# Performance work log

Hardware: AMD Instinct MI355X
Metric: run time of the kernel (lower is better)

The kernel has to match this reference:

```python
import jax, jax.numpy as jnp
import numpy as np

B, S, D, H = 4, 2048, 1024, 16
DK = D // H  # 64


def setup_inputs() -> dict:
    key = jax.random.key(0)
    ks = jax.random.split(key, 7)
    scale = 1.0 / np.sqrt(D)
    q = jax.random.normal(ks[0], (B, S, D), dtype=jnp.float32)
    k = jax.random.normal(ks[1], (B, S, D), dtype=jnp.float32)
    v = jax.random.normal(ks[2], (B, S, D), dtype=jnp.float32)
    # causal mask, broadcastable to [B, H, S, S]
    mask = jnp.tril(jnp.ones((S, S), dtype=jnp.int32))[None, None, :, :]
    Wq = jax.random.normal(ks[3], (D, D), dtype=jnp.float32) * scale
    Wk = jax.random.normal(ks[4], (D, D), dtype=jnp.float32) * scale
    Wv = jax.random.normal(ks[5], (D, D), dtype=jnp.float32) * scale
    Wo = jax.random.normal(ks[6], (D, D), dtype=jnp.float32) * scale
    return {"q": q, "k": k, "v": v, "mask": mask,
            "Wq": Wq, "Wk": Wk, "Wv": Wv, "Wo": Wo}


def reference(q, k, v, mask, Wq, Wk, Wv, Wo):
    # nn.Linear(bias=False): y = x @ W.T
    query = jnp.einsum('bsd,ed->bse', q, Wq).reshape(B, S, H, DK).transpose(0, 2, 1, 3)
    key_ = jnp.einsum('bsd,ed->bse', k, Wk).reshape(B, S, H, DK).transpose(0, 2, 1, 3)
    value = jnp.einsum('bsd,ed->bse', v, Wv).reshape(B, S, H, DK).transpose(0, 2, 1, 3)
    scores = jnp.einsum('bhqd,bhkd->bhqk', query, key_) / jnp.sqrt(jnp.float32(DK))
    scores = jnp.where(mask == 0, -jnp.inf, scores)
    probs = jax.nn.softmax(scores, axis=-1)
    x = jnp.einsum('bhqk,bhkd->bhqd', probs, value)  # [B,H,S,DK]
    x = x.transpose(0, 2, 1, 3).reshape(B, S, D)
    return jnp.einsum('bsd,ed->bse', x, Wo)
```

## Files before the change

### kernel.cpp

```cpp
#include <hip/hip_runtime.h>
#include <hip/hip_bf16.h>

constexpr int Bn = 4, Sn = 2048, Dn = 1024, Hn = 16, DKn = 64;
constexpr int Mrows = Bn * Sn;
constexpr int NQB = Sn / 64;

typedef __attribute__((ext_vector_type(8))) short short8;
typedef __attribute__((ext_vector_type(4))) float f32x4;
typedef __attribute__((ext_vector_type(4))) unsigned int u32x4;

#define DEV __device__ __forceinline__

DEV unsigned short f2bf(float f) {
    unsigned u = __builtin_bit_cast(unsigned, f);
    u += 0x7FFFu + ((u >> 16) & 1u);
    return (unsigned short)(u >> 16);
}
DEV unsigned pk2(float a, float b) {
    __hip_bfloat162 h = __float22bfloat162_rn(float2{a, b});
    unsigned u;
    __builtin_memcpy(&u, &h, 4);
    return u;
}
DEV float exp2a(float x) {
    float r;
    asm("v_exp_f32 %0, %1" : "=v"(r) : "v"(x));
    return r;
}

__global__ __launch_bounds__(256) void cvt_w(const float* __restrict__ W0,
                                             const float* __restrict__ W1,
                                             const float* __restrict__ W2,
                                             const float* __restrict__ W3,
                                             unsigned short* __restrict__ Out) {
    const float* src = blockIdx.y == 0 ? W0
                     : blockIdx.y == 1 ? W1
                     : blockIdx.y == 2 ? W2 : W3;
    size_t off = ((size_t)blockIdx.x * 256 + threadIdx.x) * 8;
    const float4* s = (const float4*)(src + off);
    float4 a = s[0], b = s[1];
    u32x4 p = {pk2(a.x, a.y), pk2(a.z, a.w), pk2(b.x, b.y), pk2(b.z, b.w)};
    *(u32x4*)(Out + (size_t)blockIdx.y * (Dn * Dn) + off) = p;
}

template <bool ABF16, bool BBF16, bool OUTF32>
DEV void gemm_body(const void* __restrict__ Ap, const void* __restrict__ Bw,
                   void* __restrict__ Out) {
    __shared__ alignas(16) unsigned short As[128 * 40];
    __shared__ alignas(16) unsigned short Bs[128 * 40];

    const int tid = threadIdx.x;
    const int bid = (int)(blockIdx.y * gridDim.x + blockIdx.x);
    const int xcd = bid & 7;
    const int jj = bid >> 3;
    const int m0 = (xcd + ((jj & 7) << 3)) * 128;
    const int n0 = (jj >> 3) * 128;
    const int lane = tid & 63;
    const int w = tid >> 6;
    const int wm = (w >> 1) * 64, wn = (w & 1) * 64;
    const int g = lane >> 4, q15 = lane & 15;

    f32x4 acc[4][4] = {};

    const int srow = tid >> 1, shalf = tid & 1;

    const float* Af = (const float*)Ap;
    const unsigned short* Ab = (const unsigned short*)Ap;
    const float* Bf = (const float*)Bw;
    const unsigned short* Bb = (const unsigned short*)Bw;

    float4 fa0, fa1, fa2, fa3, fb0, fb1, fb2, fb3;
    u32x4 ua0, ua1, ub0, ub1;

    auto loadA = [&](int kk) {
        if constexpr (ABF16) {
            const u32x4* s =
                (const u32x4*)(Ab + (size_t)(m0 + srow) * Dn + kk + shalf * 16);
            ua0 = s[0];
            ua1 = s[1];
        } else {
            const float4* s =
                (const float4*)(Af + (size_t)(m0 + srow) * Dn + kk + shalf * 16);
            fa0 = s[0]; fa1 = s[1]; fa2 = s[2]; fa3 = s[3];
        }
    };
    auto loadB = [&](int kk) {
        if constexpr (BBF16) {
            const u32x4* s =
                (const u32x4*)(Bb + (size_t)(n0 + srow) * Dn + kk + shalf * 16);
            ub0 = s[0];
            ub1 = s[1];
        } else {
            const float4* s =
                (const float4*)(Bf + (size_t)(n0 + srow) * Dn + kk + shalf * 16);
            fb0 = s[0]; fb1 = s[1]; fb2 = s[2]; fb3 = s[3];
        }
    };
    auto store = [&]() {
        u32x4* da = (u32x4*)(&As[srow * 40 + shalf * 16]);
        if constexpr (ABF16) {
            da[0] = ua0;
            da[1] = ua1;
        } else {
            u32x4 p0 = {pk2(fa0.x, fa0.y), pk2(fa0.z, fa0.w), pk2(fa1.x, fa1.y),
                        pk2(fa1.z, fa1.w)};
            u32x4 p1 = {pk2(fa2.x, fa2.y), pk2(fa2.z, fa2.w), pk2(fa3.x, fa3.y),
                        pk2(fa3.z, fa3.w)};
            da[0] = p0;
            da[1] = p1;
        }
        u32x4* db = (u32x4*)(&Bs[srow * 40 + shalf * 16]);
        if constexpr (BBF16) {
            db[0] = ub0;
            db[1] = ub1;
        } else {
            u32x4 q0 = {pk2(fb0.x, fb0.y), pk2(fb0.z, fb0.w), pk2(fb1.x, fb1.y),
                        pk2(fb1.z, fb1.w)};
            u32x4 q1 = {pk2(fb2.x, fb2.y), pk2(fb2.z, fb2.w), pk2(fb3.x, fb3.y),
                        pk2(fb3.z, fb3.w)};
            db[0] = q0;
            db[1] = q1;
        }
    };

    loadA(0);
    loadB(0);
    for (int kk = 0; kk < Dn; kk += 32) {
        store();
        __syncthreads();
        if (kk + 32 < Dn) {
            loadA(kk + 32);
            loadB(kk + 32);
        }

        short8 af[4], bf[4];
#pragma unroll
        for (int mf = 0; mf < 4; ++mf)
            af[mf] = __builtin_bit_cast(
                short8, *(const u32x4*)(&As[(wm + mf * 16 + q15) * 40 + g * 8]));
#pragma unroll
        for (int nf = 0; nf < 4; ++nf)
            bf[nf] = __builtin_bit_cast(
                short8, *(const u32x4*)(&Bs[(wn + nf * 16 + q15) * 40 + g * 8]));
#pragma unroll
        for (int mf = 0; mf < 4; ++mf)
#pragma unroll
            for (int nf = 0; nf < 4; ++nf)
                acc[mf][nf] = __builtin_amdgcn_mfma_f32_16x16x32_bf16(
                    af[mf], bf[nf], acc[mf][nf], 0, 0, 0);
        __syncthreads();
    }

#pragma unroll
    for (int mf = 0; mf < 4; ++mf)
#pragma unroll
        for (int nf = 0; nf < 4; ++nf)
#pragma unroll
            for (int r = 0; r < 4; ++r) {
                int m = m0 + wm + mf * 16 + 4 * g + r;
                int n = n0 + wn + nf * 16 + q15;
                float val = acc[mf][nf][r];
                if (OUTF32) {
                    ((float*)Out)[(size_t)m * Dn + n] = val;
                } else {
                    int b = m >> 11, s = m & (Sn - 1);
                    int h = n >> 6, dk = n & 63;
                    ((unsigned short*)Out)[(((size_t)(b * Hn + h) * Sn + s) << 6) +
                                           dk] = f2bf(val);
                }
            }
}

template <bool ABF16, bool BBF16, bool OUTF32>
__global__ __launch_bounds__(256) void gemm_nt(const void* __restrict__ Ap,
                                               const void* __restrict__ Bw,
                                               void* __restrict__ Out) {
    gemm_body<ABF16, BBF16, OUTF32>(Ap, Bw, Out);
}

__global__ __launch_bounds__(256) void attn_fwd(
    const unsigned short* __restrict__ Qb, const unsigned short* __restrict__ Kb,
    const unsigned short* __restrict__ Vb, unsigned short* __restrict__ Xb) {
    __shared__ alignas(16) unsigned short Kt[64 * 64];
    __shared__ alignas(16) unsigned short Vt[64 * 64];

    constexpr float SCL = 0.18033688f;

    const int tid = threadIdx.x;
    const int pair = blockIdx.x;
    const int bh = blockIdx.y;
    const int b = bh >> 4, h = bh & 15;
    const int lane = tid & 63, w = tid >> 6;
    const int g = lane >> 4, q15 = lane & 15;

    const unsigned short* Qh = Qb + (size_t)bh * Sn * DKn;
    const unsigned short* Kh = Kb + (size_t)bh * Sn * DKn;
    const unsigned short* Vh = Vb + (size_t)bh * Sn * DKn;

    const int st_row = tid >> 2, st_seg = tid & 3;
    const int sv_kv = tid & 63, sv_g = tid >> 6;
    const int sel = sv_kv & 1;
    const int kv_even = sv_kv & ~1;
    const unsigned kvp = (unsigned)(((kv_even & 32) | ((kv_even & 12) << 1) |
                                     ((kv_even & 16) >> 2) | (kv_even & 3)) *
                                    2);

    u32x4 kr0, kr1, vr0, vr1;
    auto load_kv = [&](int j) {
        kr0 = *(const u32x4*)(Kh + (size_t)(j * 64 + st_row) * DKn + st_seg * 8);
        kr1 = *(const u32x4*)(Kh + (size_t)(j * 64 + st_row) * DKn +
                              (st_seg + 4) * 8);
        vr0 = *(const u32x4*)(Vh + (size_t)(j * 64 + sv_kv) * DKn + sv_g * 8);
        vr1 = *(const u32x4*)(Vh + (size_t)(j * 64 + sv_kv) * DKn + sv_g * 8 + 32);
    };

    for (int hp = 0; hp < 2; ++hp) {
        const int qblk = hp == 0 ? (NQB - 1 - pair) : pair;
        const int qg = qblk * 64 + w * 16 + q15;

        short8 qf[2];
#pragma unroll
        for (int ks = 0; ks < 2; ++ks)
            qf[ks] = __builtin_bit_cast(
                short8, *(const u32x4*)(Qh + (size_t)qg * DKn + ks * 32 + g * 8));

        f32x4 xacc[4] = {};
        float m_run = -1e30f, l_run = 0.f;

        load_kv(0);
        for (int j = 0; j <= qblk; ++j) {
            {
                unsigned b0 = ((unsigned)(st_row * 128 + st_seg * 16)) ^
                              ((unsigned)(st_row & 7) << 4);
                unsigned b1 = ((unsigned)(st_row * 128 + (st_seg + 4) * 16)) ^
                              ((unsigned)(st_row & 7) << 4);
                *(u32x4*)((char*)Kt + b0) = kr0;
                *(u32x4*)((char*)Kt + b1) = kr1;
            }
#pragma unroll
            for (int r2 = 0; r2 < 2; ++r2) {
                u32x4 vvec = r2 ? vr1 : vr0;
                int dk0 = sv_g * 8 + r2 * 32;
#pragma unroll
                for (int i = 0; i < 4; ++i) {
                    unsigned mine = vvec[i];
                    unsigned theirs = (unsigned)__shfl_xor((int)mine, 1);
                    int dk_abs = dk0 + 2 * i + sel;
                    unsigned out = sel ? ((theirs >> 16) | (mine & 0xffff0000u))
                                       : ((mine & 0xffffu) | (theirs << 16));
                    unsigned byteoff = ((unsigned)(dk_abs * 128) + kvp) ^
                                       ((unsigned)(dk_abs & 7) << 4);
                    *(unsigned*)((char*)Vt + byteoff) = out;
                }
            }
            __syncthreads();

            if (j < qblk) load_kv(j + 1);

            f32x4 sacc[4] = {};
#pragma unroll
            for (int mf = 0; mf < 4; ++mf) {
                int row = mf * 16 + q15;
#pragma unroll
                for (int ks = 0; ks < 2; ++ks) {
                    unsigned byteoff = ((unsigned)(row * 128 + ks * 64 + g * 16)) ^
                                       ((unsigned)(row & 7) << 4);
                    short8 kf = __builtin_bit_cast(
                        short8, *(const u32x4*)((char*)Kt + byteoff));
                    sacc[mf] = __builtin_amdgcn_mfma_f32_16x16x32_bf16(
                        kf, qf[ks], sacc[mf], 0, 0, 0);
                }
            }

            float p[4][4];
            float pmax = -1e30f;
            const bool diag = (j == qblk);
#pragma unroll
            for (int mf = 0; mf < 4; ++mf)
#pragma unroll
                for (int r = 0; r < 4; ++r) {
                    float sv = sacc[mf][r] * SCL;
                    if (diag) {
                        int kvg = j * 64 + mf * 16 + 4 * g + r;
                        if (kvg > qg) sv = -1e30f;
                    }
                    p[mf][r] = sv;
                    pmax = fmaxf(pmax, sv);
                }
            pmax = fmaxf(pmax, __shfl_xor(pmax, 16));
            pmax = fmaxf(pmax, __shfl_xor(pmax, 32));
            if (__any(pmax > m_run + 8.f)) {
                float mnew = fmaxf(m_run, pmax);
                float corr = exp2a(m_run - mnew);
                l_run *= corr;
#pragma unroll
                for (int mf = 0; mf < 4; ++mf)
#pragma unroll
                    for (int r = 0; r < 4; ++r) xacc[mf][r] *= corr;
                m_run = mnew;
            }
            float lsum = 0.f;
#pragma unroll
            for (int mf = 0; mf < 4; ++mf)
#pragma unroll
                for (int r = 0; r < 4; ++r) {
                    float e = exp2a(p[mf][r] - m_run);
                    p[mf][r] = e;
                    lsum += e;
                }
            lsum += __shfl_xor(lsum, 16);
            lsum += __shfl_xor(lsum, 32);
            l_run += lsum;

            unsigned pkk[4][2];
#pragma unroll
            for (int mf = 0; mf < 4; ++mf) {
                pkk[mf][0] = pk2(p[mf][0], p[mf][1]);
                pkk[mf][1] = pk2(p[mf][2], p[mf][3]);
            }
#pragma unroll
            for (int ks = 0; ks < 2; ++ks) {
                u32x4 tmp = {pkk[2 * ks][0], pkk[2 * ks][1], pkk[2 * ks + 1][0],
                             pkk[2 * ks + 1][1]};
                short8 pb = __builtin_bit_cast(short8, tmp);
#pragma unroll
                for (int mf = 0; mf < 4; ++mf) {
                    int row = mf * 16 + q15;
                    unsigned byteoff = ((unsigned)(row * 128 + ks * 64 + g * 16)) ^
                                       ((unsigned)(row & 7) << 4);
                    short8 vf = __builtin_bit_cast(
                        short8, *(const u32x4*)((char*)Vt + byteoff));
                    xacc[mf] = __builtin_amdgcn_mfma_f32_16x16x32_bf16(
                        vf, pb, xacc[mf], 0, 0, 0);
                }
            }
            __syncthreads();
        }

        float inv = 1.0f / l_run;
        size_t rowbase = (size_t)(b * Sn + qblk * 64 + w * 16 + q15) * Dn + h * 64;
#pragma unroll
        for (int mf = 0; mf < 4; ++mf) {
            unsigned w0 = pk2(xacc[mf][0] * inv, xacc[mf][1] * inv);
            unsigned w1 = pk2(xacc[mf][2] * inv, xacc[mf][3] * inv);
            uint2 val = {w0, w1};
            *(uint2*)(Xb + rowbase + mf * 16 + 4 * g) = val;
        }
    }
}

extern "C" void kernel_launch(void* const* d_in, const int* in_sizes, int n_in,
                              void* d_out, int out_size, void* d_ws, size_t ws_size,
                              hipStream_t stream) {
    (void)in_sizes; (void)n_in; (void)out_size;
    const float* q = (const float*)d_in[0];
    const float* k = (const float*)d_in[1];
    const float* v = (const float*)d_in[2];
    const float* Wq = (const float*)d_in[4];
    const float* Wk = (const float*)d_in[5];
    const float* Wv = (const float*)d_in[6];
    const float* Wo = (const float*)d_in[7];

    unsigned short* Qb = (unsigned short*)d_ws;
    unsigned short* Kb = Qb + (size_t)Mrows * Dn;
    unsigned short* Vb = Kb + (size_t)Mrows * Dn;
    unsigned short* Xb = Vb + (size_t)Mrows * Dn;
    unsigned short* Wb = Xb + (size_t)Mrows * Dn;

    const size_t needW =
        (size_t)4 * Mrows * Dn * 2 + (size_t)4 * Dn * Dn * 2;
    const bool useWb = ws_size >= needW;

    dim3 blk(256);
    dim3 ggrid(Dn / 128, Mrows / 128);

    if (useWb) {
        cvt_w<<<dim3(Dn * Dn / (256 * 8), 4), blk, 0, stream>>>(Wq, Wk, Wv, Wo, Wb);
        const unsigned short* Wqb = Wb;
        const unsigned short* Wkb = Wb + (size_t)Dn * Dn;
        const unsigned short* Wvb = Wb + (size_t)2 * Dn * Dn;
        const unsigned short* Wob = Wb + (size_t)3 * Dn * Dn;
        gemm_nt<false, true, false><<<ggrid, blk, 0, stream>>>(q, Wqb, Qb);
        gemm_nt<false, true, false><<<ggrid, blk, 0, stream>>>(k, Wkb, Kb);
        gemm_nt<false, true, false><<<ggrid, blk, 0, stream>>>(v, Wvb, Vb);
        attn_fwd<<<dim3(NQB / 2, Bn * Hn), blk, 0, stream>>>(Qb, Kb, Vb, Xb);
        gemm_nt<true, true, true><<<ggrid, blk, 0, stream>>>(Xb, Wob, d_out);
    } else {
        gemm_nt<false, false, false><<<ggrid, blk, 0, stream>>>(q, Wq, Qb);
        gemm_nt<false, false, false><<<ggrid, blk, 0, stream>>>(k, Wk, Kb);
        gemm_nt<false, false, false><<<ggrid, blk, 0, stream>>>(v, Wv, Vb);
        attn_fwd<<<dim3(NQB / 2, Bn * Hn), blk, 0, stream>>>(Qb, Kb, Vb, Xb);
        gemm_nt<true, false, true><<<ggrid, blk, 0, stream>>>(Xb, Wo, d_out);
    }
}
```

Before: 228.0 us.

## Launch one attention block per query tile with interleaved ordering and setprio

Replaces the two-tiles-per-block pairing with one query tile per block, doubling the attention grid and mapping block index to query tiles in a heavy-to-light interleaved order to balance causal work. Adds s_setprio around the MFMA sections so matrix work gets issue priority, and moves the softmax scale multiply after the max reduction. The aim is more parallelism and better CU occupancy, at the cost of relying on the hardware scheduler rather than explicit pairing to balance the uneven causal workload.

```diff
diff --git a/kernel.cpp b/kernel.cpp
--- a/kernel.cpp
+++ b/kernel.cpp
@@ -187,7 +187,9 @@
     constexpr float SCL = 0.18033688f;
 
     const int tid = threadIdx.x;
-    const int pair = blockIdx.x;
+    const int xb = blockIdx.x;
+    const int c = xb & 7, t = xb >> 3;
+    const int qblk = t == 0 ? (31 - c) : t == 1 ? (16 + c) : t == 2 ? (15 - c) : c;
     const int bh = blockIdx.y;
     const int b = bh >> 4, h = bh & 15;
     const int lane = tid & 63, w = tid >> 6;
@@ -214,138 +216,140 @@
         vr1 = *(const u32x4*)(Vh + (size_t)(j * 64 + sv_kv) * DKn + sv_g * 8 + 32);
     };
 
-    for (int hp = 0; hp < 2; ++hp) {
-        const int qblk = hp == 0 ? (NQB - 1 - pair) : pair;
-        const int qg = qblk * 64 + w * 16 + q15;
-
-        short8 qf[2];
-#pragma unroll
-        for (int ks = 0; ks < 2; ++ks)
-            qf[ks] = __builtin_bit_cast(
-                short8, *(const u32x4*)(Qh + (size_t)qg * DKn + ks * 32 + g * 8));
-
-        f32x4 xacc[4] = {};
-        float m_run = -1e30f, l_run = 0.f;
-
-        load_kv(0);
-        for (int j = 0; j <= qblk; ++j) {
-            {
-                unsigned b0 = ((unsigned)(st_row * 128 + st_seg * 16)) ^
-                              ((unsigned)(st_row & 7) << 4);
-                unsigned b1 = ((unsigned)(st_row * 128 + (st_seg + 4) * 16)) ^
-                              ((unsigned)(st_row & 7) << 4);
-                *(u32x4*)((char*)Kt + b0) = kr0;
-                *(u32x4*)((char*)Kt + b1) = kr1;
-            }
-#pragma unroll
-            for (int r2 = 0; r2 < 2; ++r2) {
-                u32x4 vvec = r2 ? vr1 : vr0;
-                int dk0 = sv_g * 8 + r2 * 32;
-#pragma unroll
-                for (int i = 0; i < 4; ++i) {
-                    unsigned mine = vvec[i];
-                    unsigned theirs = (unsigned)__shfl_xor((int)mine, 1);
-                    int dk_abs = dk0 + 2 * i + sel;
-                    unsigned out = sel ? ((theirs >> 16) | (mine & 0xffff0000u))
-                                       : ((mine & 0xffffu) | (theirs << 16));
-                    unsigned byteoff = ((unsigned)(dk_abs * 128) + kvp) ^
-                                       ((unsigned)(dk_abs & 7) << 4);
-                    *(unsigned*)((char*)Vt + byteoff) = out;
+    const int qg = qblk * 64 + w * 16 + q15;
+
+    short8 qf[2];
+#pragma unroll
+    for (int ks = 0; ks < 2; ++ks)
+        qf[ks] = __builtin_bit_cast(
+            short8, *(const u32x4*)(Qh + (size_t)qg * DKn + ks * 32 + g * 8));
+
+    f32x4 xacc[4] = {};
+    float m_run = -1e30f, l_run = 0.f;
+
+    load_kv(0);
+    for (int j = 0; j <= qblk; ++j) {
+        {
+            unsigned b0 = ((unsigned)(st_row * 128 + st_seg * 16)) ^
+                          ((unsigned)(st_row & 7) << 4);
+            unsigned b1 = ((unsigned)(st_row * 128 + (st_seg + 4) * 16)) ^
+                          ((unsigned)(st_row & 7) << 4);
+            *(u32x4*)((char*)Kt + b0) = kr0;
+            *(u32x4*)((char*)Kt + b1) = kr1;
+        }
+#pragma unroll
+        for (int r2 = 0; r2 < 2; ++r2) {
+            u32x4 vvec = r2 ? vr1 : vr0;
+            int dk0 = sv_g * 8 + r2 * 32;
+#pragma unroll
+            for (int i = 0; i < 4; ++i) {
+                unsigned mine = vvec[i];
+                unsigned theirs = (unsigned)__shfl_xor((int)mine, 1);
+                int dk_abs = dk0 + 2 * i + sel;
+                unsigned out = sel ? ((theirs >> 16) | (mine & 0xffff0000u))
+                                   : ((mine & 0xffffu) | (theirs << 16));
+                unsigned byteoff = ((unsigned)(dk_abs * 128) + kvp) ^
+                                   ((unsigned)(dk_abs & 7) << 4);
+                *(unsigned*)((char*)Vt + byteoff) = out;
+            }
+        }
+        __syncthreads();
+
+        if (j < qblk) load_kv(j + 1);
+
+        f32x4 sacc[4] = {};
+        __builtin_amdgcn_s_setprio(1);
+#pragma unroll
+        for (int mf = 0; mf < 4; ++mf) {
+            int row = mf * 16 + q15;
+#pragma unroll
+            for (int ks = 0; ks < 2; ++ks) {
+                unsigned byteoff = ((unsigned)(row * 128 + ks * 64 + g * 16)) ^
+                                   ((unsigned)(row & 7) << 4);
+                short8 kf =
+                    __builtin_bit_cast(short8, *(const u32x4*)((char*)Kt + byteoff));
+                sacc[mf] = __builtin_amdgcn_mfma_f32_16x16x32_bf16(kf, qf[ks],
+                                                                   sacc[mf], 0, 0, 0);
+            }
+        }
+        __builtin_amdgcn_s_setprio(0);
+
+        float p[4][4];
+        float pmax = -1e30f;
+        const bool diag = (j == qblk);
+#pragma unroll
+        for (int mf = 0; mf < 4; ++mf)
+#pragma unroll
+            for (int r = 0; r < 4; ++r) {
+                float sv = sacc[mf][r];
+                if (diag) {
+                    int kvg = j * 64 + mf * 16 + 4 * g + r;
+                    if (kvg > qg) sv = -1e30f;
                 }
-            }
-            __syncthreads();
-
-            if (j < qblk) load_kv(j + 1);
-
-            f32x4 sacc[4] = {};
+                p[mf][r] = sv;
+                pmax = fmaxf(pmax, sv);
+            }
+        pmax = fmaxf(pmax, __shfl_xor(pmax, 16));
+        pmax = fmaxf(pmax, __shfl_xor(pmax, 32));
+        float pmax_s = pmax * SCL;
+        if (__any(pmax_s > m_run + 8.f)) {
+            float mnew = fmaxf(m_run, pmax_s);
+            float corr = exp2a(m_run - mnew);
+            l_run *= corr;
+#pragma unroll
+            for (int mf = 0; mf < 4; ++mf)
+#pragma unroll
+                for (int r = 0; r < 4; ++r) xacc[mf][r] *= corr;
+            m_run = mnew;
+        }
+        float lsum = 0.f;
+#pragma unroll
+        for (int mf = 0; mf < 4; ++mf)
+#pragma unroll
+            for (int r = 0; r < 4; ++r) {
+                float e = exp2a(p[mf][r] * SCL - m_run);
+                p[mf][r] = e;
+                lsum += e;
+            }
+        lsum += __shfl_xor(lsum, 16);
+        lsum += __shfl_xor(lsum, 32);
+        l_run += lsum;
+
+        unsigned pkk[4][2];
+#pragma unroll
+        for (int mf = 0; mf < 4; ++mf) {
+            pkk[mf][0] = pk2(p[mf][0], p[mf][1]);
+            pkk[mf][1] = pk2(p[mf][2], p[mf][3]);
+        }
+        __builtin_amdgcn_s_setprio(1);
+#pragma unroll
+        for (int ks = 0; ks < 2; ++ks) {
+            u32x4 tmp = {pkk[2 * ks][0], pkk[2 * ks][1], pkk[2 * ks + 1][0],
+                         pkk[2 * ks + 1][1]};
+            short8 pb = __builtin_bit_cast(short8, tmp);
 #pragma unroll
             for (int mf = 0; mf < 4; ++mf) {
                 int row = mf * 16 + q15;
-#pragma unroll
-                for (int ks = 0; ks < 2; ++ks) {
-                    unsigned byteoff = ((unsigned)(row * 128 + ks * 64 + g * 16)) ^
-                                       ((unsigned)(row & 7) << 4);
-                    short8 kf = __builtin_bit_cast(
-                        short8, *(const u32x4*)((char*)Kt + byteoff));
-                    sacc[mf] = __builtin_amdgcn_mfma_f32_16x16x32_bf16(
-                        kf, qf[ks], sacc[mf], 0, 0, 0);
-                }
-            }
-
-            float p[4][4];
-            float pmax = -1e30f;
-            const bool diag = (j == qblk);
-#pragma unroll
-            for (int mf = 0; mf < 4; ++mf)
-#pragma unroll
-                for (int r = 0; r < 4; ++r) {
-                    float sv = sacc[mf][r] * SCL;
-                    if (diag) {
-                        int kvg = j * 64 + mf * 16 + 4 * g + r;
-                        if (kvg > qg) sv = -1e30f;
-                    }
-                    p[mf][r] = sv;
-                    pmax = fmaxf(pmax, sv);
-                }
-            pmax = fmaxf(pmax, __shfl_xor(pmax, 16));
-            pmax = fmaxf(pmax, __shfl_xor(pmax, 32));
-            if (__any(pmax > m_run + 8.f)) {
-                float mnew = fmaxf(m_run, pmax);
-                float corr = exp2a(m_run - mnew);
-                l_run *= corr;
-#pragma unroll
-                for (int mf = 0; mf < 4; ++mf)
-#pragma unroll
-                    for (int r = 0; r < 4; ++r) xacc[mf][r] *= corr;
-                m_run = mnew;
-            }
-            float lsum = 0.f;
-#pragma unroll
-            for (int mf = 0; mf < 4; ++mf)
-#pragma unroll
-                for (int r = 0; r < 4; ++r) {
-                    float e = exp2a(p[mf][r] - m_run);
-                    p[mf][r] = e;
-                    lsum += e;
-                }
-            lsum += __shfl_xor(lsum, 16);
-            lsum += __shfl_xor(lsum, 32);
-            l_run += lsum;
-
-            unsigned pkk[4][2];
-#pragma unroll
-            for (int mf = 0; mf < 4; ++mf) {
-                pkk[mf][0] = pk2(p[mf][0], p[mf][1]);
-                pkk[mf][1] = pk2(p[mf][2], p[mf][3]);
-            }
-#pragma unroll
-            for (int ks = 0; ks < 2; ++ks) {
-                u32x4 tmp = {pkk[2 * ks][0], pkk[2 * ks][1], pkk[2 * ks + 1][0],
-                             pkk[2 * ks + 1][1]};
-                short8 pb = __builtin_bit_cast(short8, tmp);
-#pragma unroll
-                for (int mf = 0; mf < 4; ++mf) {
-                    int row = mf * 16 + q15;
-                    unsigned byteoff = ((unsigned)(row * 128 + ks * 64 + g * 16)) ^
-                                       ((unsigned)(row & 7) << 4);
-                    short8 vf = __builtin_bit_cast(
-                        short8, *(const u32x4*)((char*)Vt + byteoff));
-                    xacc[mf] = __builtin_amdgcn_mfma_f32_16x16x32_bf16(
-                        vf, pb, xacc[mf], 0, 0, 0);
-                }
-            }
-            __syncthreads();
-        }
-
-        float inv = 1.0f / l_run;
-        size_t rowbase = (size_t)(b * Sn + qblk * 64 + w * 16 + q15) * Dn + h * 64;
-#pragma unroll
-        for (int mf = 0; mf < 4; ++mf) {
-            unsigned w0 = pk2(xacc[mf][0] * inv, xacc[mf][1] * inv);
-            unsigned w1 = pk2(xacc[mf][2] * inv, xacc[mf][3] * inv);
-            uint2 val = {w0, w1};
-            *(uint2*)(Xb + rowbase + mf * 16 + 4 * g) = val;
-        }
+                unsigned byteoff = ((unsigned)(row * 128 + ks * 64 + g * 16)) ^
+                                   ((unsigned)(row & 7) << 4);
+                short8 vf =
+                    __builtin_bit_cast(short8, *(const u32x4*)((char*)Vt + byteoff));
+                xacc[mf] = __builtin_amdgcn_mfma_f32_16x16x32_bf16(vf, pb,
+                                                                   xacc[mf], 0, 0, 0);
+            }
+        }
+        __builtin_amdgcn_s_setprio(0);
+        __syncthreads();
+    }
+
+    float inv = 1.0f / l_run;
+    size_t rowbase = (size_t)(b * Sn + qblk * 64 + w * 16 + q15) * Dn + h * 64;
+#pragma unroll
+    for (int mf = 0; mf < 4; ++mf) {
+        unsigned w0 = pk2(xacc[mf][0] * inv, xacc[mf][1] * inv);
+        unsigned w1 = pk2(xacc[mf][2] * inv, xacc[mf][3] * inv);
+        uint2 val = {w0, w1};
+        *(uint2*)(Xb + rowbase + mf * 16 + 4 * g) = val;
     }
 }
 
@@ -383,13 +387,13 @@
         gemm_nt<false, true, false><<<ggrid, blk, 0, stream>>>(q, Wqb, Qb);
         gemm_nt<false, true, false><<<ggrid, blk, 0, stream>>>(k, Wkb, Kb);
         gemm_nt<false, true, false><<<ggrid, blk, 0, stream>>>(v, Wvb, Vb);
-        attn_fwd<<<dim3(NQB / 2, Bn * Hn), blk, 0, stream>>>(Qb, Kb, Vb, Xb);
+        attn_fwd<<<dim3(NQB, Bn * Hn), blk, 0, stream>>>(Qb, Kb, Vb, Xb);
         gemm_nt<true, true, true><<<ggrid, blk, 0, stream>>>(Xb, Wob, d_out);
     } else {
         gemm_nt<false, false, false><<<ggrid, blk, 0, stream>>>(q, Wq, Qb);
         gemm_nt<false, false, false><<<ggrid, blk, 0, stream>>>(k, Wk, Kb);
         gemm_nt<false, false, false><<<ggrid, blk, 0, stream>>>(v, Wv, Vb);
-        attn_fwd<<<dim3(NQB / 2, Bn * Hn), blk, 0, stream>>>(Qb, Kb, Vb, Xb);
+        attn_fwd<<<dim3(NQB, Bn * Hn), blk, 0, stream>>>(Qb, Kb, Vb, Xb);
         gemm_nt<true, false, true><<<ggrid, blk, 0, stream>>>(Xb, Wo, d_out);
     }
 }
```

After: 277.6 us. 21.8% more time.
